# Kernel optimization log

Measured on AMD Instinct MI355X. Metric: run time of the kernel, lower is better.

The kernel has to match this reference:

```python
import jax, jax.numpy as jnp
import numpy as np

B, H, T, D = 4, 16, 2048, 64


def setup_inputs() -> dict:
    key = jax.random.key(0)
    kq, kk, kv = jax.random.split(key, 3)
    q = jax.random.normal(kq, (B, H, T, D), dtype=jnp.float32)
    k = jax.random.normal(kk, (B, H, T, D), dtype=jnp.float32)
    v = jax.random.normal(kv, (B, H, T, D), dtype=jnp.float32)
    return {"q": q, "k": k, "v": v}


def reference(q, k, v):
    # scores: [B,H,T,T] = q @ k^T (no softmax, linear attention)
    scores = jnp.einsum("bhtd,bhsd->bhts", q, k)
    # causal multiplicative mask: lower-triangular ones (zero out future keys)
    t = q.shape[-2]
    causal = jnp.tril(jnp.ones((t, t), dtype=scores.dtype))  # [T,T]
    scores = scores * causal  # broadcast over [B,H]
    # output: [B,H,T,D] = masked_scores @ v
    return jnp.einsum("bhts,bhsd->bhtd", scores, v)
```

## Files before the change

kernel.cpp:

```cpp
#include <hip/hip_runtime.h>
#include <hip/hip_bf16.h>


#define T_   2048
#define D_   64
#define CCH  256
#define NCH  8
#define LW   72

typedef __bf16 bf16x8 __attribute__((ext_vector_type(8)));
typedef float  f32x4  __attribute__((ext_vector_type(4)));


__device__ inline bf16x8 pack8(float4 a, float4 b) {
  bf16x8 r;
  r[0] = (__bf16)a.x; r[1] = (__bf16)a.y; r[2] = (__bf16)a.z; r[3] = (__bf16)a.w;
  r[4] = (__bf16)b.x; r[5] = (__bf16)b.y; r[6] = (__bf16)b.z; r[7] = (__bf16)b.w;
  return r;
}

__global__ __launch_bounds__(256, 2) void state_kernel(
    const float* __restrict__ k, const float* __restrict__ v,
    float* __restrict__ kvws) {
  __shared__ __align__(16) __bf16 KT[64][LW];
  __shared__ __align__(16) __bf16 VT[64][LW];

  const int tid  = threadIdx.x;
  const int lane = tid & 63;
  const int w    = tid >> 6;
  const int quad = lane >> 4;
  const int l15  = lane & 15;
  const int bh   = blockIdx.x >> 3;
  const int c    = blockIdx.x & (NCH - 1);
  if (c == NCH - 1) return;
  const long base = ((long)bh * T_ + (long)c * CCH) * D_;
  const int d0   = w * 16;

  const f32x4 vzero = {0.f, 0.f, 0.f, 0.f};
  f32x4 st[4];
#pragma unroll
  for (int n = 0; n < 4; ++n) st[n] = vzero;

  for (int j = 0; j < 4; ++j) {
    if (j) __syncthreads();
    {
      const float* krow = k + base + (long)(j * 64 + lane) * D_ + d0;
      const float* vrow = v + base + (long)(j * 64 + lane) * D_ + d0;
      float4 k0 = *(const float4*)(krow + 0),  k1 = *(const float4*)(krow + 4);
      float4 k2 = *(const float4*)(krow + 8),  k3 = *(const float4*)(krow + 12);
      float4 v0 = *(const float4*)(vrow + 0),  v1 = *(const float4*)(vrow + 4);
      float4 v2 = *(const float4*)(vrow + 8),  v3 = *(const float4*)(vrow + 12);
      KT[d0 +  0][lane] = (__bf16)k0.x; KT[d0 +  1][lane] = (__bf16)k0.y;
      KT[d0 +  2][lane] = (__bf16)k0.z; KT[d0 +  3][lane] = (__bf16)k0.w;
      KT[d0 +  4][lane] = (__bf16)k1.x; KT[d0 +  5][lane] = (__bf16)k1.y;
      KT[d0 +  6][lane] = (__bf16)k1.z; KT[d0 +  7][lane] = (__bf16)k1.w;
      KT[d0 +  8][lane] = (__bf16)k2.x; KT[d0 +  9][lane] = (__bf16)k2.y;
      KT[d0 + 10][lane] = (__bf16)k2.z; KT[d0 + 11][lane] = (__bf16)k2.w;
      KT[d0 + 12][lane] = (__bf16)k3.x; KT[d0 + 13][lane] = (__bf16)k3.y;
      KT[d0 + 14][lane] = (__bf16)k3.z; KT[d0 + 15][lane] = (__bf16)k3.w;
      VT[d0 +  0][lane] = (__bf16)v0.x; VT[d0 +  1][lane] = (__bf16)v0.y;
      VT[d0 +  2][lane] = (__bf16)v0.z; VT[d0 +  3][lane] = (__bf16)v0.w;
      VT[d0 +  4][lane] = (__bf16)v1.x; VT[d0 +  5][lane] = (__bf16)v1.y;
      VT[d0 +  6][lane] = (__bf16)v1.z; VT[d0 +  7][lane] = (__bf16)v1.w;
      VT[d0 +  8][lane] = (__bf16)v2.x; VT[d0 +  9][lane] = (__bf16)v2.y;
      VT[d0 + 10][lane] = (__bf16)v2.z; VT[d0 + 11][lane] = (__bf16)v2.w;
      VT[d0 + 12][lane] = (__bf16)v3.x; VT[d0 + 13][lane] = (__bf16)v3.y;
      VT[d0 + 14][lane] = (__bf16)v3.z; VT[d0 + 15][lane] = (__bf16)v3.w;
    }
    __syncthreads();
    bf16x8 ka0 = *(const bf16x8*)&KT[d0 + l15][quad * 8];
    bf16x8 ka1 = *(const bf16x8*)&KT[d0 + l15][32 + quad * 8];
#pragma unroll
    for (int n = 0; n < 4; ++n) {
      bf16x8 b0 = *(const bf16x8*)&VT[n * 16 + l15][quad * 8];
      bf16x8 b1 = *(const bf16x8*)&VT[n * 16 + l15][32 + quad * 8];
      st[n] = __builtin_amdgcn_mfma_f32_16x16x32_bf16(ka0, b0, st[n], 0, 0, 0);
      st[n] = __builtin_amdgcn_mfma_f32_16x16x32_bf16(ka1, b1, st[n], 0, 0, 0);
    }
  }
  float* wsp = kvws + ((long)blockIdx.x << 12);
#pragma unroll
  for (int n = 0; n < 4; ++n)
#pragma unroll
    for (int rr = 0; rr < 4; ++rr)
      wsp[(d0 + quad * 4 + rr) * 64 + n * 16 + l15] = st[n][rr];
}

__global__ __launch_bounds__(256, 2) void attn_kernel(
    const float* __restrict__ q, const float* __restrict__ k,
    const float* __restrict__ v, const float* __restrict__ kvws,
    float* __restrict__ out) {
  __shared__ __align__(16) __bf16 Kj[64][LW];
  __shared__ __align__(16) __bf16 VT[64][LW];
  __shared__ __align__(16) __bf16 KVT[64][LW];
  __shared__ __align__(16) __bf16 Sw[4][16][LW];

  const int tid  = threadIdx.x;
  const int lane = tid & 63;
  const int w    = tid >> 6;
  const int quad = lane >> 4;
  const int l15  = lane & 15;
  const int bh   = blockIdx.x >> 3;
  const int c    = blockIdx.x & (NCH - 1);
  const long base = ((long)bh * T_ + (long)c * CCH) * D_;
  const int d0   = w * 16;

  bf16x8 qf[4][2];
#pragma unroll
  for (int i = 0; i < 4; ++i) {
    const float* qp = q + base + (long)((w + 4 * i) * 16 + l15) * D_ + quad * 8;
#pragma unroll
    for (int ks = 0; ks < 2; ++ks)
      qf[i][ks] = pack8(*(const float4*)(qp + ks * 32),
                        *(const float4*)(qp + ks * 32 + 4));
  }

  float kvacc[16];
#pragma unroll
  for (int i = 0; i < 16; ++i) kvacc[i] = 0.f;
  {
    const float* wsbh = kvws + ((long)(bh * NCH) << 12);
    for (int cc = 0; cc < c; ++cc) {
      const float* p = wsbh + ((long)cc << 12) + d0 * 64 + lane;
#pragma unroll
      for (int i = 0; i < 16; ++i) kvacc[i] += p[i * 64];
    }
  }

  {
    const float* krow = k + base + (long)lane * D_ + d0;
    const float* vrow = v + base + (long)lane * D_ + d0;
    float4 k0 = *(const float4*)(krow + 0),  k1 = *(const float4*)(krow + 4);
    float4 k2 = *(const float4*)(krow + 8),  k3 = *(const float4*)(krow + 12);
    float4 v0 = *(const float4*)(vrow + 0),  v1 = *(const float4*)(vrow + 4);
    float4 v2 = *(const float4*)(vrow + 8),  v3 = *(const float4*)(vrow + 12);
    *(bf16x8*)&Kj[lane][d0]     = pack8(k0, k1);
    *(bf16x8*)&Kj[lane][d0 + 8] = pack8(k2, k3);
    VT[d0 +  0][lane] = (__bf16)v0.x; VT[d0 +  1][lane] = (__bf16)v0.y;
    VT[d0 +  2][lane] = (__bf16)v0.z; VT[d0 +  3][lane] = (__bf16)v0.w;
    VT[d0 +  4][lane] = (__bf16)v1.x; VT[d0 +  5][lane] = (__bf16)v1.y;
    VT[d0 +  6][lane] = (__bf16)v1.z; VT[d0 +  7][lane] = (__bf16)v1.w;
    VT[d0 +  8][lane] = (__bf16)v2.x; VT[d0 +  9][lane] = (__bf16)v2.y;
    VT[d0 + 10][lane] = (__bf16)v2.z; VT[d0 + 11][lane] = (__bf16)v2.w;
    VT[d0 + 12][lane] = (__bf16)v3.x; VT[d0 + 13][lane] = (__bf16)v3.y;
    VT[d0 + 14][lane] = (__bf16)v3.z; VT[d0 + 15][lane] = (__bf16)v3.w;
  }
  {
    float4 a0 = {kvacc[0], kvacc[1], kvacc[2], kvacc[3]};
    float4 a1 = {kvacc[4], kvacc[5], kvacc[6], kvacc[7]};
    float4 a2 = {kvacc[8], kvacc[9], kvacc[10], kvacc[11]};
    float4 a3 = {kvacc[12], kvacc[13], kvacc[14], kvacc[15]};
    *(bf16x8*)&KVT[lane][d0]     = pack8(a0, a1);
    *(bf16x8*)&KVT[lane][d0 + 8] = pack8(a2, a3);
  }

  const f32x4 vzero = {0.f, 0.f, 0.f, 0.f};
  f32x4 acc[4][4];
#pragma unroll
  for (int i = 0; i < 4; ++i)
#pragma unroll
    for (int n = 0; n < 4; ++n) acc[i][n] = vzero;

  __syncthreads();

#pragma unroll
  for (int ks = 0; ks < 2; ++ks)
#pragma unroll
    for (int n = 0; n < 4; ++n) {
      bf16x8 b = *(const bf16x8*)&KVT[n * 16 + l15][ks * 32 + quad * 8];
#pragma unroll
      for (int i = 0; i < 4; ++i)
        acc[i][n] =
            __builtin_amdgcn_mfma_f32_16x16x32_bf16(qf[i][ks], b, acc[i][n], 0, 0, 0);
    }

  for (int j = 0; j < 4; ++j) {
    if (j) {
      __syncthreads();
      const float* krow = k + base + (long)(j * 64 + lane) * D_ + d0;
      const float* vrow = v + base + (long)(j * 64 + lane) * D_ + d0;
      float4 k0 = *(const float4*)(krow + 0),  k1 = *(const float4*)(krow + 4);
      float4 k2 = *(const float4*)(krow + 8),  k3 = *(const float4*)(krow + 12);
      float4 v0 = *(const float4*)(vrow + 0),  v1 = *(const float4*)(vrow + 4);
      float4 v2 = *(const float4*)(vrow + 8),  v3 = *(const float4*)(vrow + 12);
      *(bf16x8*)&Kj[lane][d0]     = pack8(k0, k1);
      *(bf16x8*)&Kj[lane][d0 + 8] = pack8(k2, k3);
      VT[d0 +  0][lane] = (__bf16)v0.x; VT[d0 +  1][lane] = (__bf16)v0.y;
      VT[d0 +  2][lane] = (__bf16)v0.z; VT[d0 +  3][lane] = (__bf16)v0.w;
      VT[d0 +  4][lane] = (__bf16)v1.x; VT[d0 +  5][lane] = (__bf16)v1.y;
      VT[d0 +  6][lane] = (__bf16)v1.z; VT[d0 +  7][lane] = (__bf16)v1.w;
      VT[d0 +  8][lane] = (__bf16)v2.x; VT[d0 +  9][lane] = (__bf16)v2.y;
      VT[d0 + 10][lane] = (__bf16)v2.z; VT[d0 + 11][lane] = (__bf16)v2.w;
      VT[d0 + 12][lane] = (__bf16)v3.x; VT[d0 + 13][lane] = (__bf16)v3.y;
      VT[d0 + 14][lane] = (__bf16)v3.z; VT[d0 + 15][lane] = (__bf16)v3.w;
      __syncthreads();
    }

    bf16x8 vb[2][4];
#pragma unroll
    for (int ks = 0; ks < 2; ++ks)
#pragma unroll
      for (int n = 0; n < 4; ++n)
        vb[ks][n] = *(const bf16x8*)&VT[n * 16 + l15][ks * 32 + quad * 8];

    for (int i = j; i < 4; ++i) {
      f32x4 s4[4];
#pragma unroll
      for (int n = 0; n < 4; ++n) s4[n] = vzero;
#pragma unroll
      for (int ks = 0; ks < 2; ++ks)
#pragma unroll
        for (int n = 0; n < 4; ++n) {
          bf16x8 b = *(const bf16x8*)&Kj[n * 16 + l15][ks * 32 + quad * 8];
          s4[n] = __builtin_amdgcn_mfma_f32_16x16x32_bf16(qf[i][ks], b, s4[n], 0, 0, 0);
        }
#pragma unroll
      for (int n = 0; n < 4; ++n)
#pragma unroll
        for (int rr = 0; rr < 4; ++rr) {
          float val = s4[n][rr];
          if (i == j && (n * 16 + l15 > 16 * w + quad * 4 + rr)) val = 0.f;
          Sw[w][quad * 4 + rr][n * 16 + l15] = (__bf16)val;
        }
      bf16x8 a0 = *(const bf16x8*)&Sw[w][l15][quad * 8];
      bf16x8 a1 = *(const bf16x8*)&Sw[w][l15][32 + quad * 8];
#pragma unroll
      for (int n = 0; n < 4; ++n) {
        acc[i][n] = __builtin_amdgcn_mfma_f32_16x16x32_bf16(a0, vb[0][n], acc[i][n], 0, 0, 0);
        acc[i][n] = __builtin_amdgcn_mfma_f32_16x16x32_bf16(a1, vb[1][n], acc[i][n], 0, 0, 0);
      }
    }
  }

  float* op = out + base;
#pragma unroll
  for (int i = 0; i < 4; ++i) {
    int row = (w + 4 * i) * 16 + quad * 4;
#pragma unroll
    for (int n = 0; n < 4; ++n)
#pragma unroll
      for (int rr = 0; rr < 4; ++rr)
        op[(long)(row + rr) * D_ + n * 16 + l15] = acc[i][n][rr];
  }
}

extern "C" void kernel_launch(void* const* d_in, const int* in_sizes, int n_in,
                              void* d_out, int out_size, void* d_ws, size_t ws_size,
                              hipStream_t stream) {
  const float* q = (const float*)d_in[0];
  const float* k = (const float*)d_in[1];
  const float* v = (const float*)d_in[2];
  float* out = (float*)d_out;
  float* kvws = (float*)d_ws;

  hipLaunchKernelGGL(state_kernel, dim3(512), dim3(256), 0, stream, k, v, kvws);
  hipLaunchKernelGGL(attn_kernel, dim3(512), dim3(256), 0, stream,
                     q, k, v, kvws, out);
}
```

Baseline: 162.8 us.

## Halve chunk size to 128, store chunk states in bf16, unroll intra-chunk loop

Splits each sequence into 16 chunks of 128 instead of 8 of 256, doubling the block count to 1024 and raising launch bounds to 4 blocks per CU for more parallelism. Per-chunk KV states are written to the workspace as bf16 in a transposed layout, and the prefix sum unpacks bf16 pairs from 32-bit words, halving workspace traffic. The intra-chunk loop over two 64-row tiles is unrolled by hand and the scratch buffers are merged to cut shared memory. The trade-off is a longer serial prefix reduction per block (up to 15 chunk states) and bf16 rounding of the stored partial states.

```diff
diff --git a/kernel.cpp b/kernel.cpp
--- a/kernel.cpp
+++ b/kernel.cpp
@@ -4,12 +4,15 @@
 
 #define T_   2048
 #define D_   64
-#define CCH  256
-#define NCH  8
+#define CCH  128
+#define NCH  16
 #define LW   72
 
 typedef __bf16 bf16x8 __attribute__((ext_vector_type(8)));
+typedef __bf16 bf16x4 __attribute__((ext_vector_type(4)));
+typedef __bf16 bf16x2 __attribute__((ext_vector_type(2)));
 typedef float  f32x4  __attribute__((ext_vector_type(4)));
+typedef unsigned int u32;
 
 
 __device__ inline bf16x8 pack8(float4 a, float4 b) {
@@ -19,9 +22,9 @@
   return r;
 }
 
-__global__ __launch_bounds__(256, 2) void state_kernel(
+__global__ __launch_bounds__(256, 4) void state_kernel(
     const float* __restrict__ k, const float* __restrict__ v,
-    float* __restrict__ kvws) {
+    __bf16* __restrict__ stws) {
   __shared__ __align__(16) __bf16 KT[64][LW];
   __shared__ __align__(16) __bf16 VT[64][LW];
 
@@ -30,8 +33,8 @@
   const int w    = tid >> 6;
   const int quad = lane >> 4;
   const int l15  = lane & 15;
-  const int bh   = blockIdx.x >> 3;
-  const int c    = blockIdx.x & (NCH - 1);
+  const int bh   = (int)blockIdx.x >> 4;
+  const int c    = (int)blockIdx.x & (NCH - 1);
   if (c == NCH - 1) return;
   const long base = ((long)bh * T_ + (long)c * CCH) * D_;
   const int d0   = w * 16;
@@ -41,7 +44,7 @@
 #pragma unroll
   for (int n = 0; n < 4; ++n) st[n] = vzero;
 
-  for (int j = 0; j < 4; ++j) {
+  for (int j = 0; j < 2; ++j) {
     if (j) __syncthreads();
     {
       const float* krow = k + base + (long)(j * 64 + lane) * D_ + d0;
@@ -78,53 +81,42 @@
       st[n] = __builtin_amdgcn_mfma_f32_16x16x32_bf16(ka1, b1, st[n], 0, 0, 0);
     }
   }
-  float* wsp = kvws + ((long)blockIdx.x << 12);
-#pragma unroll
-  for (int n = 0; n < 4; ++n)
-#pragma unroll
-    for (int rr = 0; rr < 4; ++rr)
-      wsp[(d0 + quad * 4 + rr) * 64 + n * 16 + l15] = st[n][rr];
+  __bf16* wsp = stws + ((long)blockIdx.x << 12);
+#pragma unroll
+  for (int n = 0; n < 4; ++n) {
+    bf16x4 pk;
+    pk[0] = (__bf16)st[n][0]; pk[1] = (__bf16)st[n][1];
+    pk[2] = (__bf16)st[n][2]; pk[3] = (__bf16)st[n][3];
+    *(bf16x4*)&wsp[(n * 16 + l15) * 64 + d0 + quad * 4] = pk;
+  }
 }
 
-__global__ __launch_bounds__(256, 2) void attn_kernel(
+__global__ __launch_bounds__(256, 4) void attn_kernel(
     const float* __restrict__ q, const float* __restrict__ k,
-    const float* __restrict__ v, const float* __restrict__ kvws,
+    const float* __restrict__ v, const __bf16* __restrict__ stws,
     float* __restrict__ out) {
   __shared__ __align__(16) __bf16 Kj[64][LW];
   __shared__ __align__(16) __bf16 VT[64][LW];
-  __shared__ __align__(16) __bf16 KVT[64][LW];
-  __shared__ __align__(16) __bf16 Sw[4][16][LW];
+  __shared__ __align__(16) __bf16 Ubuf[2 * 64 * LW];
 
   const int tid  = threadIdx.x;
   const int lane = tid & 63;
   const int w    = tid >> 6;
   const int quad = lane >> 4;
   const int l15  = lane & 15;
-  const int bh   = blockIdx.x >> 3;
-  const int c    = blockIdx.x & (NCH - 1);
+  const int bh   = (int)blockIdx.x >> 4;
+  const int c    = (int)blockIdx.x & (NCH - 1);
   const long base = ((long)bh * T_ + (long)c * CCH) * D_;
   const int d0   = w * 16;
 
-  bf16x8 qf[4][2];
-#pragma unroll
-  for (int i = 0; i < 4; ++i) {
+  bf16x8 qf[2][2];
+#pragma unroll
+  for (int i = 0; i < 2; ++i) {
     const float* qp = q + base + (long)((w + 4 * i) * 16 + l15) * D_ + quad * 8;
 #pragma unroll
     for (int ks = 0; ks < 2; ++ks)
       qf[i][ks] = pack8(*(const float4*)(qp + ks * 32),
                         *(const float4*)(qp + ks * 32 + 4));
-  }
-
-  float kvacc[16];
-#pragma unroll
-  for (int i = 0; i < 16; ++i) kvacc[i] = 0.f;
-  {
-    const float* wsbh = kvws + ((long)(bh * NCH) << 12);
-    for (int cc = 0; cc < c; ++cc) {
-      const float* p = wsbh + ((long)cc << 12) + d0 * 64 + lane;
-#pragma unroll
-      for (int i = 0; i < 16; ++i) kvacc[i] += p[i * 64];
-    }
   }
 
   {
@@ -145,19 +137,36 @@
     VT[d0 + 12][lane] = (__bf16)v3.x; VT[d0 + 13][lane] = (__bf16)v3.y;
     VT[d0 + 14][lane] = (__bf16)v3.z; VT[d0 + 15][lane] = (__bf16)v3.w;
   }
-  {
-    float4 a0 = {kvacc[0], kvacc[1], kvacc[2], kvacc[3]};
-    float4 a1 = {kvacc[4], kvacc[5], kvacc[6], kvacc[7]};
-    float4 a2 = {kvacc[8], kvacc[9], kvacc[10], kvacc[11]};
-    float4 a3 = {kvacc[12], kvacc[13], kvacc[14], kvacc[15]};
-    *(bf16x8*)&KVT[lane][d0]     = pack8(a0, a1);
-    *(bf16x8*)&KVT[lane][d0 + 8] = pack8(a2, a3);
+
+  float2 kv2[8];
+#pragma unroll
+  for (int t = 0; t < 8; ++t) { kv2[t].x = 0.f; kv2[t].y = 0.f; }
+  {
+    const u32* wsb = (const u32*)stws + ((long)(bh * NCH) << 11);
+    for (int cc = 0; cc < c; ++cc) {
+      const u32* p = wsb + ((long)cc << 11) + w * 512 + lane;
+#pragma unroll
+      for (int t = 0; t < 8; ++t) {
+        u32 u = p[t * 64];
+        kv2[t].x += __uint_as_float(u << 16);
+        kv2[t].y += __uint_as_float(u & 0xffff0000u);
+      }
+    }
+  }
+  {
+    const int h = lane >> 5, l31 = lane & 31;
+#pragma unroll
+    for (int t = 0; t < 8; ++t) {
+      bf16x2 pr;
+      pr[0] = (__bf16)kv2[t].x; pr[1] = (__bf16)kv2[t].y;
+      *(bf16x2*)&Ubuf[(16 * w + 2 * t + h) * LW + 2 * l31] = pr;
+    }
   }
 
   const f32x4 vzero = {0.f, 0.f, 0.f, 0.f};
-  f32x4 acc[4][4];
-#pragma unroll
-  for (int i = 0; i < 4; ++i)
+  f32x4 acc[2][4];
+#pragma unroll
+  for (int i = 0; i < 2; ++i)
 #pragma unroll
     for (int n = 0; n < 4; ++n) acc[i][n] = vzero;
 
@@ -167,74 +176,122 @@
   for (int ks = 0; ks < 2; ++ks)
 #pragma unroll
     for (int n = 0; n < 4; ++n) {
-      bf16x8 b = *(const bf16x8*)&KVT[n * 16 + l15][ks * 32 + quad * 8];
-#pragma unroll
-      for (int i = 0; i < 4; ++i)
-        acc[i][n] =
-            __builtin_amdgcn_mfma_f32_16x16x32_bf16(qf[i][ks], b, acc[i][n], 0, 0, 0);
-    }
-
-  for (int j = 0; j < 4; ++j) {
-    if (j) {
-      __syncthreads();
-      const float* krow = k + base + (long)(j * 64 + lane) * D_ + d0;
-      const float* vrow = v + base + (long)(j * 64 + lane) * D_ + d0;
-      float4 k0 = *(const float4*)(krow + 0),  k1 = *(const float4*)(krow + 4);
-      float4 k2 = *(const float4*)(krow + 8),  k3 = *(const float4*)(krow + 12);
-      float4 v0 = *(const float4*)(vrow + 0),  v1 = *(const float4*)(vrow + 4);
-      float4 v2 = *(const float4*)(vrow + 8),  v3 = *(const float4*)(vrow + 12);
-      *(bf16x8*)&Kj[lane][d0]     = pack8(k0, k1);
-      *(bf16x8*)&Kj[lane][d0 + 8] = pack8(k2, k3);
-      VT[d0 +  0][lane] = (__bf16)v0.x; VT[d0 +  1][lane] = (__bf16)v0.y;
-      VT[d0 +  2][lane] = (__bf16)v0.z; VT[d0 +  3][lane] = (__bf16)v0.w;
-      VT[d0 +  4][lane] = (__bf16)v1.x; VT[d0 +  5][lane] = (__bf16)v1.y;
-      VT[d0 +  6][lane] = (__bf16)v1.z; VT[d0 +  7][lane] = (__bf16)v1.w;
-      VT[d0 +  8][lane] = (__bf16)v2.x; VT[d0 +  9][lane] = (__bf16)v2.y;
-      VT[d0 + 10][lane] = (__bf16)v2.z; VT[d0 + 11][lane] = (__bf16)v2.w;
-      VT[d0 + 12][lane] = (__bf16)v3.x; VT[d0 + 13][lane] = (__bf16)v3.y;
-      VT[d0 + 14][lane] = (__bf16)v3.z; VT[d0 + 15][lane] = (__bf16)v3.w;
-      __syncthreads();
-    }
-
-    bf16x8 vb[2][4];
-#pragma unroll
-    for (int ks = 0; ks < 2; ++ks)
-#pragma unroll
-      for (int n = 0; n < 4; ++n)
-        vb[ks][n] = *(const bf16x8*)&VT[n * 16 + l15][ks * 32 + quad * 8];
-
-    for (int i = j; i < 4; ++i) {
-      f32x4 s4[4];
-#pragma unroll
-      for (int n = 0; n < 4; ++n) s4[n] = vzero;
-#pragma unroll
-      for (int ks = 0; ks < 2; ++ks)
-#pragma unroll
-        for (int n = 0; n < 4; ++n) {
-          bf16x8 b = *(const bf16x8*)&Kj[n * 16 + l15][ks * 32 + quad * 8];
-          s4[n] = __builtin_amdgcn_mfma_f32_16x16x32_bf16(qf[i][ks], b, s4[n], 0, 0, 0);
-        }
-#pragma unroll
-      for (int n = 0; n < 4; ++n)
-#pragma unroll
-        for (int rr = 0; rr < 4; ++rr) {
-          float val = s4[n][rr];
-          if (i == j && (n * 16 + l15 > 16 * w + quad * 4 + rr)) val = 0.f;
-          Sw[w][quad * 4 + rr][n * 16 + l15] = (__bf16)val;
-        }
-      bf16x8 a0 = *(const bf16x8*)&Sw[w][l15][quad * 8];
-      bf16x8 a1 = *(const bf16x8*)&Sw[w][l15][32 + quad * 8];
-#pragma unroll
-      for (int n = 0; n < 4; ++n) {
-        acc[i][n] = __builtin_amdgcn_mfma_f32_16x16x32_bf16(a0, vb[0][n], acc[i][n], 0, 0, 0);
-        acc[i][n] = __builtin_amdgcn_mfma_f32_16x16x32_bf16(a1, vb[1][n], acc[i][n], 0, 0, 0);
-      }
+      bf16x8 b = *(const bf16x8*)&Ubuf[(n * 16 + l15) * LW + ks * 32 + quad * 8];
+      acc[0][n] = __builtin_amdgcn_mfma_f32_16x16x32_bf16(qf[0][ks], b, acc[0][n], 0, 0, 0);
+      acc[1][n] = __builtin_amdgcn_mfma_f32_16x16x32_bf16(qf[1][ks], b, acc[1][n], 0, 0, 0);
+    }
+
+  bf16x8 vb[2][4];
+#pragma unroll
+  for (int ks = 0; ks < 2; ++ks)
+#pragma unroll
+    for (int n = 0; n < 4; ++n)
+      vb[ks][n] = *(const bf16x8*)&VT[n * 16 + l15][ks * 32 + quad * 8];
+
+  f32x4 sA[4], sB[4];
+#pragma unroll
+  for (int n = 0; n < 4; ++n) { sA[n] = vzero; sB[n] = vzero; }
+#pragma unroll
+  for (int ks = 0; ks < 2; ++ks)
+#pragma unroll
+    for (int n = 0; n < 4; ++n) {
+      bf16x8 bK = *(const bf16x8*)&Kj[n * 16 + l15][ks * 32 + quad * 8];
+      sA[n] = __builtin_amdgcn_mfma_f32_16x16x32_bf16(qf[0][ks], bK, sA[n], 0, 0, 0);
+      sB[n] = __builtin_amdgcn_mfma_f32_16x16x32_bf16(qf[1][ks], bK, sB[n], 0, 0, 0);
+    }
+
+  __syncthreads();
+
+  __bf16* sw0 = &Ubuf[((w * 2 + 0) * 16) * LW];
+  __bf16* sw1 = &Ubuf[((w * 2 + 1) * 16) * LW];
+
+#pragma unroll
+  for (int n = 0; n < 4; ++n)
+#pragma unroll
+    for (int rr = 0; rr < 4; ++rr) {
+      float val = sA[n][rr];
+      if (n * 16 + l15 > 16 * w + quad * 4 + rr) val = 0.f;
+      sw0[(quad * 4 + rr) * LW + n * 16 + l15] = (__bf16)val;
+    }
+#pragma unroll
+  for (int n = 0; n < 4; ++n)
+#pragma unroll
+    for (int rr = 0; rr < 4; ++rr)
+      sw1[(quad * 4 + rr) * LW + n * 16 + l15] = (__bf16)sB[n][rr];
+
+  {
+    bf16x8 a0 = *(const bf16x8*)&sw0[l15 * LW + quad * 8];
+    bf16x8 a1 = *(const bf16x8*)&sw0[l15 * LW + 32 + quad * 8];
+    bf16x8 b0 = *(const bf16x8*)&sw1[l15 * LW + quad * 8];
+    bf16x8 b1 = *(const bf16x8*)&sw1[l15 * LW + 32 + quad * 8];
+#pragma unroll
+    for (int n = 0; n < 4; ++n) {
+      acc[0][n] = __builtin_amdgcn_mfma_f32_16x16x32_bf16(a0, vb[0][n], acc[0][n], 0, 0, 0);
+      acc[0][n] = __builtin_amdgcn_mfma_f32_16x16x32_bf16(a1, vb[1][n], acc[0][n], 0, 0, 0);
+      acc[1][n] = __builtin_amdgcn_mfma_f32_16x16x32_bf16(b0, vb[0][n], acc[1][n], 0, 0, 0);
+      acc[1][n] = __builtin_amdgcn_mfma_f32_16x16x32_bf16(b1, vb[1][n], acc[1][n], 0, 0, 0);
+    }
+  }
+
+  __syncthreads();
+
+  {
+    const float* krow = k + base + (long)(64 + lane) * D_ + d0;
+    const float* vrow = v + base + (long)(64 + lane) * D_ + d0;
+    float4 k0 = *(const float4*)(krow + 0),  k1 = *(const float4*)(krow + 4);
+    float4 k2 = *(const float4*)(krow + 8),  k3 = *(const float4*)(krow + 12);
+    float4 v0 = *(const float4*)(vrow + 0),  v1 = *(const float4*)(vrow + 4);
+    float4 v2 = *(const float4*)(vrow + 8),  v3 = *(const float4*)(vrow + 12);
+    *(bf16x8*)&Kj[lane][d0]     = pack8(k0, k1);
+    *(bf16x8*)&Kj[lane][d0 + 8] = pack8(k2, k3);
+    VT[d0 +  0][lane] = (__bf16)v0.x; VT[d0 +  1][lane] = (__bf16)v0.y;
+    VT[d0 +  2][lane] = (__bf16)v0.z; VT[d0 +  3][lane] = (__bf16)v0.w;
+    VT[d0 +  4][lane] = (__bf16)v1.x; VT[d0 +  5][lane] = (__bf16)v1.y;
+    VT[d0 +  6][lane] = (__bf16)v1.z; VT[d0 +  7][lane] = (__bf16)v1.w;
+    VT[d0 +  8][lane] = (__bf16)v2.x; VT[d0 +  9][lane] = (__bf16)v2.y;
+    VT[d0 + 10][lane] = (__bf16)v2.z; VT[d0 + 11][lane] = (__bf16)v2.w;
+    VT[d0 + 12][lane] = (__bf16)v3.x; VT[d0 + 13][lane] = (__bf16)v3.y;
+    VT[d0 + 14][lane] = (__bf16)v3.z; VT[d0 + 15][lane] = (__bf16)v3.w;
+  }
+  __syncthreads();
+
+#pragma unroll
+  for (int ks = 0; ks < 2; ++ks)
+#pragma unroll
+    for (int n = 0; n < 4; ++n)
+      vb[ks][n] = *(const bf16x8*)&VT[n * 16 + l15][ks * 32 + quad * 8];
+
+  f32x4 sC[4];
+#pragma unroll
+  for (int n = 0; n < 4; ++n) sC[n] = vzero;
+#pragma unroll
+  for (int ks = 0; ks < 2; ++ks)
+#pragma unroll
+    for (int n = 0; n < 4; ++n) {
+      bf16x8 bK = *(const bf16x8*)&Kj[n * 16 + l15][ks * 32 + quad * 8];
+      sC[n] = __builtin_amdgcn_mfma_f32_16x16x32_bf16(qf[1][ks], bK, sC[n], 0, 0, 0);
+    }
+#pragma unroll
+  for (int n = 0; n < 4; ++n)
+#pragma unroll
+    for (int rr = 0; rr < 4; ++rr) {
+      float val = sC[n][rr];
+      if (n * 16 + l15 > 16 * w + quad * 4 + rr) val = 0.f;
+      sw0[(quad * 4 + rr) * LW + n * 16 + l15] = (__bf16)val;
+    }
+  {
+    bf16x8 a0 = *(const bf16x8*)&sw0[l15 * LW + quad * 8];
+    bf16x8 a1 = *(const bf16x8*)&sw0[l15 * LW + 32 + quad * 8];
+#pragma unroll
+    for (int n = 0; n < 4; ++n) {
+      acc[1][n] = __builtin_amdgcn_mfma_f32_16x16x32_bf16(a0, vb[0][n], acc[1][n], 0, 0, 0);
+      acc[1][n] = __builtin_amdgcn_mfma_f32_16x16x32_bf16(a1, vb[1][n], acc[1][n], 0, 0, 0);
     }
   }
 
   float* op = out + base;
 #pragma unroll
-  for (int i = 0; i < 4; ++i) {
+  for (int i = 0; i < 2; ++i) {
     int row = (w + 4 * i) * 16 + quad * 4;
 #pragma unroll
     for (int n = 0; n < 4; ++n)
@@ -251,9 +308,10 @@
   const float* k = (const float*)d_in[1];
   const float* v = (const float*)d_in[2];
   float* out = (float*)d_out;
-  float* kvws = (float*)d_ws;
-
-  hipLaunchKernelGGL(state_kernel, dim3(512), dim3(256), 0, stream, k, v, kvws);
-  hipLaunchKernelGGL(attn_kernel, dim3(512), dim3(256), 0, stream,
-                     q, k, v, kvws, out);
+  __bf16* stws = (__bf16*)d_ws;
+
+  hipLaunchKernelGGL(state_kernel, dim3(64 * NCH), dim3(256), 0, stream,
+                     k, v, stws);
+  hipLaunchKernelGGL(attn_kernel, dim3(64 * NCH), dim3(256), 0, stream,
+                     q, k, v, stws, out);
 }
```

Result: no change. 160.3 us (-1.6%).
